# Optimization experiments

Hardware: AMD Instinct MI355X
Metric: run time of the kernel (lower is better)

Reference implementation:

```python
import jax, jax.numpy as jnp
import numpy as np

TAU = 0.07
MARGIN = 0.2
NUM_SPECIES = 64  # matches fill_max of species_ids


def _l2norm(x):
    return x / jnp.linalg.norm(x, axis=-1, keepdims=True)


def setup_inputs() -> dict:
    key = jax.random.key(0)
    k1, k2, k3 = jax.random.split(key, 3)
    B, D = 8192, 256
    species_embed = _l2norm(jax.random.normal(k1, (B, D), dtype=jnp.float32))
    text_embed = _l2norm(jax.random.normal(k2, (B, D), dtype=jnp.float32))
    species_ids = jax.random.randint(k3, (B,), 0, NUM_SPECIES, dtype=jnp.int32)
    return {"species_embed": species_embed, "text_embed": text_embed,
            "species_ids": species_ids}


def reference(species_embed, text_embed, species_ids):
    B = species_embed.shape[0]
    dtype = species_embed.dtype

    sim = species_embed @ text_embed.T                      # (B, B)
    same = species_ids[:, None] == species_ids[None, :]     # (B, B) bool, symmetric
    diag_sim = jnp.diagonal(sim)                            # (B,)

    # ---- intra-species symmetric InfoNCE (per-species CE, averaged over species)
    logits = sim / TAU
    neg_inf = jnp.finfo(dtype).min
    masked = jnp.where(same, logits, neg_inf)               # restrict to same-species cols
    diag_logit = diag_sim / TAU
    ce_v2t = jax.scipy.special.logsumexp(masked, axis=1) - diag_logit   # per-row CE
    ce_t2v = jax.scipy.special.logsumexp(masked.T, axis=1) - diag_logit # transpose: same mask is symmetric

    ones = jnp.ones((B,), dtype=dtype)
    counts = jax.ops.segment_sum(ones, species_ids, num_segments=NUM_SPECIES)          # group sizes
    seg_v2t = jax.ops.segment_sum(ce_v2t, species_ids, num_segments=NUM_SPECIES)
    seg_t2v = jax.ops.segment_sum(ce_t2v, species_ids, num_segments=NUM_SPECIES)
    valid_s = counts >= 2                                   # groups with <2 members skipped
    per_species = (seg_v2t + seg_t2v) / (2.0 * jnp.maximum(counts, 1.0))
    n_valid = jnp.maximum(jnp.sum(valid_s.astype(dtype)), 1.0)
    loss_infonce = jnp.sum(jnp.where(valid_s, per_species, 0.0)) / n_valid

    # ---- cross-species triplet (pos = mean same-species sim excl. self, neg = mean diff-species sim)
    same_f = same.astype(dtype)
    row_same_sum = jnp.sum(sim * same_f, axis=1)            # includes diagonal
    row_sum = jnp.sum(sim, axis=1)
    pos_cnt = jnp.sum(same_f, axis=1) - 1.0
    neg_cnt = B - jnp.sum(same_f, axis=1)
    pos_mean = (row_same_sum - diag_sim) / jnp.maximum(pos_cnt, 1.0)
    neg_mean = (row_sum - row_same_sum) / jnp.maximum(neg_cnt, 1.0)
    tri = jax.nn.relu(neg_mean - pos_mean + MARGIN)
    valid_i = (pos_cnt > 0) & (neg_cnt > 0)
    n_valid_i = jnp.maximum(jnp.sum(valid_i.astype(dtype)), 1.0)
    loss_triplet = jnp.sum(jnp.where(valid_i, tri, 0.0)) / n_valid_i

    return loss_infonce + loss_triplet
```

## Files before the change

kernel.cpp:

```cpp
#include <hip/hip_runtime.h>
#include <hip/hip_fp16.h>

#define TAU 0.07f
#define MARGIN 0.2f
#define NSPEC 64
#define BB 8192
#define DD 256

#define WS_SCALARS   0
#define WS_COUNTS    64
#define WS_OFFSETS   320
#define WS_LSEROW    1024
#define WS_LSECOL    33792
#define WS_TS        66560
#define WS_T         132096
#define WS_MEMBER    133120

typedef _Float16 half8 __attribute__((ext_vector_type(8)));
typedef float float4v __attribute__((ext_vector_type(4)));
typedef unsigned int uint4v __attribute__((ext_vector_type(4)));

__device__ __forceinline__ uint4v pack8(float4 a, float4 b) {
  half8 h;
  h[0] = (_Float16)a.x; h[1] = (_Float16)a.y; h[2] = (_Float16)a.z; h[3] = (_Float16)a.w;
  h[4] = (_Float16)b.x; h[5] = (_Float16)b.y; h[6] = (_Float16)b.z; h[7] = (_Float16)b.w;
  return __builtin_bit_cast(uint4v, h);
}

__device__ __forceinline__ float dot4(float4 a, float4 b) {
  return a.x * b.x + a.y * b.y + a.z * b.z + a.w * b.w;
}

__global__ void kA(const int* __restrict__ ids, char* __restrict__ ws) {
  int bid = blockIdx.x, tid = threadIdx.x;
  if (bid == 0) {
    int* counts_g = (int*)(ws + WS_COUNTS);
    int* offsets_g = (int*)(ws + WS_OFFSETS);
    int* memberList = (int*)(ws + WS_MEMBER);
    float* scalars = (float*)(ws + WS_SCALARS);
    __shared__ int cnt[NSPEC];
    __shared__ int off[NSPEC];
    if (tid < 8) ((unsigned*)scalars)[tid] = 0u;
    if (tid < NSPEC) cnt[tid] = 0;
    __syncthreads();
    int myS[8], myP[8];
    #pragma unroll
    for (int r = 0; r < 8; ++r) {
      int i = r * 1024 + tid;
      int s = ids[i];
      myS[r] = s;
      myP[r] = atomicAdd(&cnt[s], 1);
    }
    __syncthreads();
    if (tid < NSPEC) {
      int o = 0;
      for (int t = 0; t < NSPEC; ++t) o += (t < tid) ? cnt[t] : 0;
      off[tid] = o;
      offsets_g[tid] = o;
      int c = cnt[tid];
      counts_g[tid] = c;
      unsigned long long bv = __ballot(c >= 2);
      float nvi = (c >= 2 && c <= BB - 1) ? (float)c : 0.f;
      for (int o2 = 1; o2 < 64; o2 <<= 1) nvi += __shfl_xor(nvi, o2);
      if (tid == 0) {
        scalars[2] = (float)__popcll(bv);
        scalars[3] = nvi;
      }
    }
    __syncthreads();
    #pragma unroll
    for (int r = 0; r < 8; ++r) {
      int i = r * 1024 + tid;
      memberList[off[myS[r]] + myP[r]] = i;
    }
  } else {
    int b = bid - 1;
    if (tid < 258) {
      float4v z4 = {0.f, 0.f, 0.f, 0.f};
      *(float4v*)(ws + WS_LSEROW + b * 4128 + tid * 16) = z4;
    }
  }
}

__global__ void kB(const float* __restrict__ sp, const float* __restrict__ tx,
                   const int* __restrict__ counts, const int* __restrict__ offsets,
                   const int* __restrict__ memberList,
                   float* Ts, float* T, float* lseRow, float* lseCol) {
  __shared__ uint4v frag[1536];
  __shared__ int idx[192];
  int bid = blockIdx.x;
  int tid = threadIdx.x;

  if (bid >= 1024) {
    int b = bid - 1024;
    int d = tid;
    const float* base = tx + (b * 32) * DD + d;
    float acc = 0.f;
    #pragma unroll 8
    for (int rr = 0; rr < 32; ++rr) acc += base[rr * DD];
    atomicAdd(&T[d], acc);
    return;
  }
  if (bid >= 512) {
    int v2 = bid - 512;
    int s = v2 & 63, r = v2 >> 6;
    int m = counts[s], g0 = offsets[s];
    int k0 = (m * r) >> 3, k1e = (m * (r + 1)) >> 3;
    if (k0 >= k1e) return;
    int d = tid;
    float acc = 0.f;
    int k = k0;
    for (; k + 4 <= k1e; k += 4) {
      int i0 = memberList[g0 + k];
      int i1 = memberList[g0 + k + 1];
      int i2 = memberList[g0 + k + 2];
      int i3 = memberList[g0 + k + 3];
      float a0 = tx[i0 * DD + d];
      float a1 = tx[i1 * DD + d];
      float a2 = tx[i2 * DD + d];
      float a3 = tx[i3 * DD + d];
      acc += a0 + a1 + a2 + a3;
    }
    for (; k < k1e; ++k) acc += tx[memberList[g0 + k] * DD + d];
    atomicAdd(&Ts[s * DD + d], acc);
    return;
  }

  int s = bid & 63;
  int m = counts[s];
  int g0 = offsets[s];
  int lane = tid & 63, wv = tid >> 6;
  int quad = lane >> 4, cl = lane & 15;
  int rt0 = (bid >> 6) & 3, ct0 = (bid >> 8) & 1;

  for (int rt = rt0; rt * 64 < m; rt += 4) {
    for (int ct = ct0; ct * 128 < m; ct += 2) {
      __syncthreads();
      if (tid < 192) {
        int base = (tid < 64) ? (rt * 64 + tid) : (ct * 128 + (tid - 64));
        idx[tid] = (base < m) ? memberList[g0 + base] : -1;
      }
      __syncthreads();

      const float* srcB[6];
      bool val[6];
      int dst[6];
      float4 r0[6], r1[6];
      #pragma unroll
      for (int p = 0; p < 6; ++p) {
        int u = p * 256 + tid;
        int isB = u >= 512;
        int v = isB ? (u - 512) : u;
        int row = v >> 3, sub = v & 7;
        int ksl = sub >> 2, q = sub & 3;
        int ridx = idx[isB ? (64 + row) : row];
        val[p] = ridx >= 0;
        srcB[p] = (isB ? tx : sp) + (val[p] ? ridx : 0) * DD + ksl * 32 + q * 8;
        dst[p] = isB ? (512 + (ksl * 128 + row) * 4 + q)
                     : ((ksl * 64 + row) * 4 + q);
      }
      #pragma unroll
      for (int p = 0; p < 6; ++p) {
        r0[p] = *reinterpret_cast<const float4*>(srcB[p]);
        r1[p] = *reinterpret_cast<const float4*>(srcB[p] + 4);
      }

      float4v acc[8];
      #pragma unroll
      for (int cf = 0; cf < 8; ++cf) acc[cf] = (float4v){0.f, 0.f, 0.f, 0.f};

      for (int kc = 0; kc < 4; ++kc) {
        __syncthreads();
        uint4v z4 = (uint4v){0u, 0u, 0u, 0u};
        #pragma unroll
        for (int p = 0; p < 6; ++p)
          frag[dst[p]] = val[p] ? pack8(r0[p], r1[p]) : z4;
        __syncthreads();
        if (kc < 3) {
          #pragma unroll
          for (int p = 0; p < 6; ++p) {
            r0[p] = *reinterpret_cast<const float4*>(srcB[p] + (kc + 1) * 64);
            r1[p] = *reinterpret_cast<const float4*>(srcB[p] + (kc + 1) * 64 + 4);
          }
        }
        #pragma unroll
        for (int ksl = 0; ksl < 2; ++ksl) {
          half8 a = __builtin_bit_cast(half8, frag[(ksl * 64 + wv * 16 + cl) * 4 + quad]);
          #pragma unroll
          for (int cf = 0; cf < 8; ++cf) {
            half8 b = __builtin_bit_cast(half8, frag[512 + (ksl * 128 + cf * 16 + cl) * 4 + quad]);
            acc[cf] = __builtin_amdgcn_mfma_f32_16x16x32_f16(a, b, acc[cf], 0, 0, 0);
          }
        }
      }

      int riBase = rt * 64 + wv * 16 + quad * 4;
      float rowAcc[4] = {0.f, 0.f, 0.f, 0.f};
      #pragma unroll
      for (int cf = 0; cf < 8; ++cf) {
        int ci = ct * 128 + cf * 16 + cl;
        bool cv = ci < m;
        float colAcc = 0.f;
        #pragma unroll
        for (int reg = 0; reg < 4; ++reg) {
          bool rv = (riBase + reg) < m;
          float e = (rv && cv) ? __expf(acc[cf][reg] * (1.f / TAU)) : 0.f;
          rowAcc[reg] += e;
          colAcc += e;
        }
        colAcc += __shfl_xor(colAcc, 16);
        colAcc += __shfl_xor(colAcc, 32);
        if (quad == 0 && cv) atomicAdd(&lseCol[g0 + ci], colAcc);
      }
      #pragma unroll
      for (int reg = 0; reg < 4; ++reg) {
        float v = rowAcc[reg];
        v += __shfl_xor(v, 1);
        v += __shfl_xor(v, 2);
        v += __shfl_xor(v, 4);
        v += __shfl_xor(v, 8);
        if (cl == 0 && (riBase + reg) < m) atomicAdd(&lseRow[g0 + riBase + reg], v);
      }
    }
  }
}

__global__ void kC(const float* __restrict__ sp, const float* __restrict__ tx,
                   const int* __restrict__ ids, const int* __restrict__ counts,
                   const int* __restrict__ memberList,
                   const float* __restrict__ Ts, const float* __restrict__ T,
                   const float* __restrict__ lseRow, const float* __restrict__ lseCol,
                   float* scalars, float* out) {
  __shared__ float red[32];
  int tid = threadIdx.x;
  int gt = blockIdx.x * 1024 + tid;
  int g = gt >> 6, lane = gt & 63;
  int i = memberList[g];
  int s = ids[i];
  int m = counts[s];
  float4 a = *reinterpret_cast<const float4*>(sp + i * DD + lane * 4);
  float4 b = *reinterpret_cast<const float4*>(tx + i * DD + lane * 4);
  float4 c = *reinterpret_cast<const float4*>(Ts + s * DD + lane * 4);
  float4 tv = *reinterpret_cast<const float4*>(T + lane * 4);
  float dDiag = dot4(a, b);
  float dTs   = dot4(a, c);
  float dT    = dot4(a, tv);
  #pragma unroll
  for (int o = 1; o < 64; o <<= 1) {
    dDiag += __shfl_xor(dDiag, o);
    dTs   += __shfl_xor(dTs, o);
    dT    += __shfl_xor(dT, o);
  }
  if (lane == 0) {
    float term = 0.f, tri = 0.f;
    if (m >= 2) {
      term = (__logf(lseRow[g]) + __logf(lseCol[g]) - 2.f * dDiag * (1.f / TAU)) /
             (2.f * (float)m);
      float posMean = (dTs - dDiag) / fmaxf((float)(m - 1), 1.f);
      float negMean = (dT - dTs) / fmaxf((float)(BB - m), 1.f);
      if (m <= BB - 1) tri = fmaxf(negMean - posMean + MARGIN, 0.f);
    }
    int wv = tid >> 6;
    red[wv] = term;
    red[16 + wv] = tri;
  }
  __syncthreads();
  if (tid == 0) {
    float infoS = 0.f, triS = 0.f;
    #pragma unroll
    for (int w = 0; w < 16; ++w) { infoS += red[w]; triS += red[16 + w]; }
    atomicAdd(&scalars[1], infoS);
    atomicAdd(&scalars[0], triS);
    __threadfence();
    unsigned prev = atomicAdd((unsigned*)&scalars[4], 1u);
    if (prev == (unsigned)(gridDim.x - 1)) {
      float fi = atomicAdd(&scalars[1], 0.f);
      float ft = atomicAdd(&scalars[0], 0.f);
      float nv = scalars[2];
      float nvi = scalars[3];
      out[0] = fi / fmaxf(nv, 1.f) + ft / fmaxf(nvi, 1.f);
    }
  }
}

extern "C" void kernel_launch(void* const* d_in, const int* in_sizes, int n_in,
                              void* d_out, int out_size, void* d_ws, size_t ws_size,
                              hipStream_t stream) {
  const float* sp = (const float*)d_in[0];
  const float* tx = (const float*)d_in[1];
  const int* ids = (const int*)d_in[2];
  float* out = (float*)d_out;

  char* ws = (char*)d_ws;
  float* scalars = (float*)(ws + WS_SCALARS);
  int* counts = (int*)(ws + WS_COUNTS);
  int* offsets = (int*)(ws + WS_OFFSETS);
  float* lseRow = (float*)(ws + WS_LSEROW);
  float* lseCol = (float*)(ws + WS_LSECOL);
  float* Ts = (float*)(ws + WS_TS);
  float* T = (float*)(ws + WS_T);
  int* memberList = (int*)(ws + WS_MEMBER);

  kA<<<33, 1024, 0, stream>>>(ids, ws);
  kB<<<1280, 256, 0, stream>>>(sp, tx, counts, offsets, memberList,
                               Ts, T, lseRow, lseCol);
  kC<<<512, 1024, 0, stream>>>(sp, tx, ids, counts, memberList, Ts, T,
                               lseRow, lseCol, scalars, out);
}
```

Baseline: 111.3 us.

## Fuse three kernels into one persistent megakernel with flag-based inter-block sync

Merges the histogram/member-list, zeroing, masked GEMM-LSE, species-sum, total-sum and final reduction kernels into one launch where block ranges take roles and wait on global atomic flags and counters. It aims to remove kernel launch gaps and let independent work (e.g. the total text sum) overlap with the histogram phase. In exchange it relies on spin-waiting and co-residency/forward progress of blocks, and flags persisting across calls (flag1, flagZ0 never cleared) risk races with stale state on repeated invocations.

```diff
diff --git a/kernel.cpp b/kernel.cpp
--- a/kernel.cpp
+++ b/kernel.cpp
@@ -7,14 +7,30 @@
 #define BB 8192
 #define DD 256
 
-#define WS_SCALARS   0
-#define WS_COUNTS    64
-#define WS_OFFSETS   320
-#define WS_LSEROW    1024
-#define WS_LSECOL    33792
-#define WS_TS        66560
-#define WS_T         132096
-#define WS_MEMBER    133120
+#define MAGICZ 0x51u
+#define MAGIC1 0x1357A5C3u
+
+#define B_ZERO0   1
+#define B_K5      33
+#define B_K2      545
+#define B_T       1057
+#define B_KC      1313
+#define N_WORK2   1312u
+#define N_KC      2048
+#define N_TOTAL   3361
+
+#define WS_SCALARS 0
+#define WS_COUNTS  64
+#define WS_OFFSETS 320
+#define WS_FLAGZ0  576
+#define WS_ZCNT    580
+#define WS_FLAG1   584
+#define WS_DONE2   588
+#define WS_LSEROW  1024
+#define WS_LSECOL  33792
+#define WS_TS      66560
+#define WS_T       132096
+#define WS_MEMBER  133120
 
 typedef _Float16 half8 __attribute__((ext_vector_type(8)));
 typedef float float4v __attribute__((ext_vector_type(4)));
@@ -31,34 +47,62 @@
   return a.x * b.x + a.y * b.y + a.z * b.z + a.w * b.w;
 }
 
-__global__ void kA(const int* __restrict__ ids, char* __restrict__ ws) {
+__device__ __forceinline__ unsigned aload(unsigned* p) { return atomicAdd(p, 0u); }
+
+__device__ __forceinline__ void spin1(unsigned* p, unsigned v) {
+  if (threadIdx.x == 0) {
+    while (aload(p) != v) __builtin_amdgcn_s_sleep(8);
+  }
+  __syncthreads();
+}
+__device__ __forceinline__ void spin2(unsigned* p1, unsigned v1, unsigned* p2, unsigned v2) {
+  if (threadIdx.x == 0) {
+    while (aload(p1) != v1 || aload(p2) != v2) __builtin_amdgcn_s_sleep(8);
+  }
+  __syncthreads();
+}
+
+__global__ void __launch_bounds__(256)
+mega(const float* __restrict__ sp, const float* __restrict__ tx,
+     const int* __restrict__ ids, char* __restrict__ ws, float* __restrict__ out) {
+  float* scalars = (float*)(ws + WS_SCALARS);
+  int* counts = (int*)(ws + WS_COUNTS);
+  int* offsets = (int*)(ws + WS_OFFSETS);
+  unsigned* flagZ0 = (unsigned*)(ws + WS_FLAGZ0);
+  unsigned* zcnt = (unsigned*)(ws + WS_ZCNT);
+  unsigned* flag1 = (unsigned*)(ws + WS_FLAG1);
+  unsigned* done2 = (unsigned*)(ws + WS_DONE2);
+  float* lseRow = (float*)(ws + WS_LSEROW);
+  float* lseCol = (float*)(ws + WS_LSECOL);
+  float* Ts = (float*)(ws + WS_TS);
+  float* T = (float*)(ws + WS_T);
+  int* memberList = (int*)(ws + WS_MEMBER);
+
   int bid = blockIdx.x, tid = threadIdx.x;
+
+  __shared__ union {
+    struct { int cnt[NSPEC]; int cur[NSPEC]; } h;
+    struct { uint4v frag[1536]; int idx[192]; } k5;
+    float red[8];
+  } sm;
+
   if (bid == 0) {
-    int* counts_g = (int*)(ws + WS_COUNTS);
-    int* offsets_g = (int*)(ws + WS_OFFSETS);
-    int* memberList = (int*)(ws + WS_MEMBER);
-    float* scalars = (float*)(ws + WS_SCALARS);
-    __shared__ int cnt[NSPEC];
-    __shared__ int off[NSPEC];
+    if (tid == 0) { *zcnt = 0u; *done2 = 0u; }
     if (tid < 8) ((unsigned*)scalars)[tid] = 0u;
-    if (tid < NSPEC) cnt[tid] = 0;
-    __syncthreads();
-    int myS[8], myP[8];
+    if (tid < NSPEC) sm.h.cnt[tid] = 0;
+    __threadfence();
+    __syncthreads();
+    if (tid == 0) atomicExch(flagZ0, MAGICZ);
     #pragma unroll
-    for (int r = 0; r < 8; ++r) {
-      int i = r * 1024 + tid;
-      int s = ids[i];
-      myS[r] = s;
-      myP[r] = atomicAdd(&cnt[s], 1);
-    }
+    for (int r = 0; r < 32; ++r) atomicAdd(&sm.h.cnt[ids[r * 256 + tid]], 1);
     __syncthreads();
     if (tid < NSPEC) {
       int o = 0;
-      for (int t = 0; t < NSPEC; ++t) o += (t < tid) ? cnt[t] : 0;
-      off[tid] = o;
-      offsets_g[tid] = o;
-      int c = cnt[tid];
-      counts_g[tid] = c;
+      for (int t = 0; t < NSPEC; ++t) o += (t < tid) ? sm.h.cnt[t] : 0;
+      offsets[tid] = o;
+      sm.h.cur[tid] = o;
+      int c = sm.h.cnt[tid];
+      counts[tid] = c;
       unsigned long long bv = __ballot(c >= 2);
       float nvi = (c >= 2 && c <= BB - 1) ? (float)c : 0.f;
       for (int o2 = 1; o2 < 64; o2 <<= 1) nvi += __shfl_xor(nvi, o2);
@@ -69,216 +113,223 @@
     }
     __syncthreads();
     #pragma unroll
-    for (int r = 0; r < 8; ++r) {
-      int i = r * 1024 + tid;
-      memberList[off[myS[r]] + myP[r]] = i;
-    }
-  } else {
-    int b = bid - 1;
-    if (tid < 258) {
-      float4v z4 = {0.f, 0.f, 0.f, 0.f};
-      *(float4v*)(ws + WS_LSEROW + b * 4128 + tid * 16) = z4;
-    }
-  }
-}
-
-__global__ void kB(const float* __restrict__ sp, const float* __restrict__ tx,
-                   const int* __restrict__ counts, const int* __restrict__ offsets,
-                   const int* __restrict__ memberList,
-                   float* Ts, float* T, float* lseRow, float* lseCol) {
-  __shared__ uint4v frag[1536];
-  __shared__ int idx[192];
-  int bid = blockIdx.x;
-  int tid = threadIdx.x;
-
-  if (bid >= 1024) {
-    int b = bid - 1024;
+    for (int r = 0; r < 32; ++r) {
+      int i = r * 256 + tid;
+      int s = ids[i];
+      int pos = atomicAdd(&sm.h.cur[s], 1);
+      memberList[pos] = i;
+    }
+    __threadfence();
+    __syncthreads();
+    if (tid == 0) atomicExch(flag1, MAGIC1);
+    return;
+
+  } else if (bid < B_K5) {
+    spin1(flagZ0, MAGICZ);
+    int b = bid - B_ZERO0;
+    char* base = ws + WS_LSEROW + b * 4128;
+    float4v z4 = {0.f, 0.f, 0.f, 0.f};
+    *(float4v*)(base + tid * 16) = z4;
+    if (tid < 2) *(float4v*)(base + (256 + tid) * 16) = z4;
+    __threadfence();
+    __syncthreads();
+    if (tid == 0) atomicAdd(zcnt, 1u);
+    spin1(flag1, MAGIC1);
+    if (tid == 0) atomicAdd(done2, 1u);
+    return;
+
+  } else if (bid < B_K2) {
+    int v = bid - B_K5;
+    spin2(flag1, MAGIC1, zcnt, 32u);
+    int s = v & 63;
+    int m = counts[s];
+    int g0 = offsets[s];
+    int lane = tid & 63, wv = tid >> 6;
+    int quad = lane >> 4, cl = lane & 15;
+    int rt0 = (v >> 6) & 3, ct0 = (v >> 8) & 1;
+
+    for (int rt = rt0; rt * 64 < m; rt += 4) {
+      for (int ct = ct0; ct * 128 < m; ct += 2) {
+        __syncthreads();
+        if (tid < 192) {
+          int base = (tid < 64) ? (rt * 64 + tid) : (ct * 128 + (tid - 64));
+          sm.k5.idx[tid] = (base < m) ? memberList[g0 + base] : -1;
+        }
+        __syncthreads();
+
+        const float* srcB[6];
+        bool val[6];
+        int dst[6];
+        float4 r0[6], r1[6];
+        #pragma unroll
+        for (int p = 0; p < 6; ++p) {
+          int u = p * 256 + tid;
+          int isB = u >= 512;
+          int vv = isB ? (u - 512) : u;
+          int row = vv >> 3, sub = vv & 7;
+          int ksl = sub >> 2, q = sub & 3;
+          int ridx = sm.k5.idx[isB ? (64 + row) : row];
+          val[p] = ridx >= 0;
+          srcB[p] = (isB ? tx : sp) + (val[p] ? ridx : 0) * DD + ksl * 32 + q * 8;
+          dst[p] = isB ? (512 + (ksl * 128 + row) * 4 + q)
+                       : ((ksl * 64 + row) * 4 + q);
+        }
+        #pragma unroll
+        for (int p = 0; p < 6; ++p) {
+          r0[p] = *reinterpret_cast<const float4*>(srcB[p]);
+          r1[p] = *reinterpret_cast<const float4*>(srcB[p] + 4);
+        }
+
+        float4v acc[8];
+        #pragma unroll
+        for (int cf = 0; cf < 8; ++cf) acc[cf] = (float4v){0.f, 0.f, 0.f, 0.f};
+
+        for (int kc = 0; kc < 4; ++kc) {
+          __syncthreads();
+          uint4v z4 = (uint4v){0u, 0u, 0u, 0u};
+          #pragma unroll
+          for (int p = 0; p < 6; ++p)
+            sm.k5.frag[dst[p]] = val[p] ? pack8(r0[p], r1[p]) : z4;
+          __syncthreads();
+          if (kc < 3) {
+            #pragma unroll
+            for (int p = 0; p < 6; ++p) {
+              r0[p] = *reinterpret_cast<const float4*>(srcB[p] + (kc + 1) * 64);
+              r1[p] = *reinterpret_cast<const float4*>(srcB[p] + (kc + 1) * 64 + 4);
+            }
+          }
+          #pragma unroll
+          for (int ksl = 0; ksl < 2; ++ksl) {
+            half8 a = __builtin_bit_cast(half8, sm.k5.frag[(ksl * 64 + wv * 16 + cl) * 4 + quad]);
+            #pragma unroll
+            for (int cf = 0; cf < 8; ++cf) {
+              half8 b = __builtin_bit_cast(half8, sm.k5.frag[512 + (ksl * 128 + cf * 16 + cl) * 4 + quad]);
+              acc[cf] = __builtin_amdgcn_mfma_f32_16x16x32_f16(a, b, acc[cf], 0, 0, 0);
+            }
+          }
+        }
+
+        int riBase = rt * 64 + wv * 16 + quad * 4;
+        float rowAcc[4] = {0.f, 0.f, 0.f, 0.f};
+        #pragma unroll
+        for (int cf = 0; cf < 8; ++cf) {
+          int ci = ct * 128 + cf * 16 + cl;
+          bool cv = ci < m;
+          float colAcc = 0.f;
+          #pragma unroll
+          for (int reg = 0; reg < 4; ++reg) {
+            bool rv = (riBase + reg) < m;
+            float e = (rv && cv) ? __expf(acc[cf][reg] * (1.f / TAU)) : 0.f;
+            rowAcc[reg] += e;
+            colAcc += e;
+          }
+          colAcc += __shfl_xor(colAcc, 16);
+          colAcc += __shfl_xor(colAcc, 32);
+          if (quad == 0 && cv) atomicAdd(&lseCol[g0 + ci], colAcc);
+        }
+        #pragma unroll
+        for (int reg = 0; reg < 4; ++reg) {
+          float vv = rowAcc[reg];
+          vv += __shfl_xor(vv, 1);
+          vv += __shfl_xor(vv, 2);
+          vv += __shfl_xor(vv, 4);
+          vv += __shfl_xor(vv, 8);
+          if (cl == 0 && (riBase + reg) < m) atomicAdd(&lseRow[g0 + riBase + reg], vv);
+        }
+      }
+    }
+    __threadfence();
+    __syncthreads();
+    if (tid == 0) atomicAdd(done2, 1u);
+    return;
+
+  } else if (bid < B_T) {
+    int v2 = bid - B_K2;
+    spin2(flag1, MAGIC1, zcnt, 32u);
+    int s = v2 & 63, r = v2 >> 6;
+    int m = counts[s], g0 = offsets[s];
+    int k0 = (m * r) >> 3, k1e = (m * (r + 1)) >> 3;
+    if (k0 < k1e) {
+      int d = tid;
+      float acc = 0.f;
+      int k = k0;
+      for (; k + 4 <= k1e; k += 4) {
+        int i0 = memberList[g0 + k];
+        int i1 = memberList[g0 + k + 1];
+        int i2 = memberList[g0 + k + 2];
+        int i3 = memberList[g0 + k + 3];
+        acc += tx[i0 * DD + d] + tx[i1 * DD + d] + tx[i2 * DD + d] + tx[i3 * DD + d];
+      }
+      for (; k < k1e; ++k) acc += tx[memberList[g0 + k] * DD + d];
+      atomicAdd(&Ts[s * DD + d], acc);
+    }
+    __threadfence();
+    __syncthreads();
+    if (tid == 0) atomicAdd(done2, 1u);
+    return;
+
+  } else if (bid < B_KC) {
+    int b = bid - B_T;
     int d = tid;
     const float* base = tx + (b * 32) * DD + d;
     float acc = 0.f;
     #pragma unroll 8
     for (int rr = 0; rr < 32; ++rr) acc += base[rr * DD];
+    spin2(flag1, MAGIC1, zcnt, 32u);
     atomicAdd(&T[d], acc);
+    __threadfence();
+    __syncthreads();
+    if (tid == 0) atomicAdd(done2, 1u);
     return;
   }
-  if (bid >= 512) {
-    int v2 = bid - 512;
-    int s = v2 & 63, r = v2 >> 6;
-    int m = counts[s], g0 = offsets[s];
-    int k0 = (m * r) >> 3, k1e = (m * (r + 1)) >> 3;
-    if (k0 >= k1e) return;
-    int d = tid;
-    float acc = 0.f;
-    int k = k0;
-    for (; k + 4 <= k1e; k += 4) {
-      int i0 = memberList[g0 + k];
-      int i1 = memberList[g0 + k + 1];
-      int i2 = memberList[g0 + k + 2];
-      int i3 = memberList[g0 + k + 3];
-      float a0 = tx[i0 * DD + d];
-      float a1 = tx[i1 * DD + d];
-      float a2 = tx[i2 * DD + d];
-      float a3 = tx[i3 * DD + d];
-      acc += a0 + a1 + a2 + a3;
-    }
-    for (; k < k1e; ++k) acc += tx[memberList[g0 + k] * DD + d];
-    atomicAdd(&Ts[s * DD + d], acc);
-    return;
-  }
-
-  int s = bid & 63;
-  int m = counts[s];
-  int g0 = offsets[s];
-  int lane = tid & 63, wv = tid >> 6;
-  int quad = lane >> 4, cl = lane & 15;
-  int rt0 = (bid >> 6) & 3, ct0 = (bid >> 8) & 1;
-
-  for (int rt = rt0; rt * 64 < m; rt += 4) {
-    for (int ct = ct0; ct * 128 < m; ct += 2) {
-      __syncthreads();
-      if (tid < 192) {
-        int base = (tid < 64) ? (rt * 64 + tid) : (ct * 128 + (tid - 64));
-        idx[tid] = (base < m) ? memberList[g0 + base] : -1;
-      }
-      __syncthreads();
-
-      const float* srcB[6];
-      bool val[6];
-      int dst[6];
-      float4 r0[6], r1[6];
-      #pragma unroll
-      for (int p = 0; p < 6; ++p) {
-        int u = p * 256 + tid;
-        int isB = u >= 512;
-        int v = isB ? (u - 512) : u;
-        int row = v >> 3, sub = v & 7;
-        int ksl = sub >> 2, q = sub & 3;
-        int ridx = idx[isB ? (64 + row) : row];
-        val[p] = ridx >= 0;
-        srcB[p] = (isB ? tx : sp) + (val[p] ? ridx : 0) * DD + ksl * 32 + q * 8;
-        dst[p] = isB ? (512 + (ksl * 128 + row) * 4 + q)
-                     : ((ksl * 64 + row) * 4 + q);
-      }
-      #pragma unroll
-      for (int p = 0; p < 6; ++p) {
-        r0[p] = *reinterpret_cast<const float4*>(srcB[p]);
-        r1[p] = *reinterpret_cast<const float4*>(srcB[p] + 4);
-      }
-
-      float4v acc[8];
-      #pragma unroll
-      for (int cf = 0; cf < 8; ++cf) acc[cf] = (float4v){0.f, 0.f, 0.f, 0.f};
-
-      for (int kc = 0; kc < 4; ++kc) {
-        __syncthreads();
-        uint4v z4 = (uint4v){0u, 0u, 0u, 0u};
-        #pragma unroll
-        for (int p = 0; p < 6; ++p)
-          frag[dst[p]] = val[p] ? pack8(r0[p], r1[p]) : z4;
-        __syncthreads();
-        if (kc < 3) {
-          #pragma unroll
-          for (int p = 0; p < 6; ++p) {
-            r0[p] = *reinterpret_cast<const float4*>(srcB[p] + (kc + 1) * 64);
-            r1[p] = *reinterpret_cast<const float4*>(srcB[p] + (kc + 1) * 64 + 4);
-          }
-        }
-        #pragma unroll
-        for (int ksl = 0; ksl < 2; ++ksl) {
-          half8 a = __builtin_bit_cast(half8, frag[(ksl * 64 + wv * 16 + cl) * 4 + quad]);
-          #pragma unroll
-          for (int cf = 0; cf < 8; ++cf) {
-            half8 b = __builtin_bit_cast(half8, frag[512 + (ksl * 128 + cf * 16 + cl) * 4 + quad]);
-            acc[cf] = __builtin_amdgcn_mfma_f32_16x16x32_f16(a, b, acc[cf], 0, 0, 0);
-          }
-        }
-      }
-
-      int riBase = rt * 64 + wv * 16 + quad * 4;
-      float rowAcc[4] = {0.f, 0.f, 0.f, 0.f};
-      #pragma unroll
-      for (int cf = 0; cf < 8; ++cf) {
-        int ci = ct * 128 + cf * 16 + cl;
-        bool cv = ci < m;
-        float colAcc = 0.f;
-        #pragma unroll
-        for (int reg = 0; reg < 4; ++reg) {
-          bool rv = (riBase + reg) < m;
-          float e = (rv && cv) ? __expf(acc[cf][reg] * (1.f / TAU)) : 0.f;
-          rowAcc[reg] += e;
-          colAcc += e;
-        }
-        colAcc += __shfl_xor(colAcc, 16);
-        colAcc += __shfl_xor(colAcc, 32);
-        if (quad == 0 && cv) atomicAdd(&lseCol[g0 + ci], colAcc);
-      }
-      #pragma unroll
-      for (int reg = 0; reg < 4; ++reg) {
-        float v = rowAcc[reg];
-        v += __shfl_xor(v, 1);
-        v += __shfl_xor(v, 2);
-        v += __shfl_xor(v, 4);
-        v += __shfl_xor(v, 8);
-        if (cl == 0 && (riBase + reg) < m) atomicAdd(&lseRow[g0 + riBase + reg], v);
-      }
-    }
-  }
-}
-
-__global__ void kC(const float* __restrict__ sp, const float* __restrict__ tx,
-                   const int* __restrict__ ids, const int* __restrict__ counts,
-                   const int* __restrict__ memberList,
-                   const float* __restrict__ Ts, const float* __restrict__ T,
-                   const float* __restrict__ lseRow, const float* __restrict__ lseCol,
-                   float* scalars, float* out) {
-  __shared__ float red[32];
-  int tid = threadIdx.x;
-  int gt = blockIdx.x * 1024 + tid;
-  int g = gt >> 6, lane = gt & 63;
-  int i = memberList[g];
-  int s = ids[i];
-  int m = counts[s];
-  float4 a = *reinterpret_cast<const float4*>(sp + i * DD + lane * 4);
-  float4 b = *reinterpret_cast<const float4*>(tx + i * DD + lane * 4);
-  float4 c = *reinterpret_cast<const float4*>(Ts + s * DD + lane * 4);
-  float4 tv = *reinterpret_cast<const float4*>(T + lane * 4);
-  float dDiag = dot4(a, b);
-  float dTs   = dot4(a, c);
-  float dT    = dot4(a, tv);
-  #pragma unroll
-  for (int o = 1; o < 64; o <<= 1) {
-    dDiag += __shfl_xor(dDiag, o);
-    dTs   += __shfl_xor(dTs, o);
-    dT    += __shfl_xor(dT, o);
-  }
-  if (lane == 0) {
-    float term = 0.f, tri = 0.f;
-    if (m >= 2) {
-      term = (__logf(lseRow[g]) + __logf(lseCol[g]) - 2.f * dDiag * (1.f / TAU)) /
-             (2.f * (float)m);
-      float posMean = (dTs - dDiag) / fmaxf((float)(m - 1), 1.f);
-      float negMean = (dT - dTs) / fmaxf((float)(BB - m), 1.f);
-      if (m <= BB - 1) tri = fmaxf(negMean - posMean + MARGIN, 0.f);
-    }
-    int wv = tid >> 6;
-    red[wv] = term;
-    red[16 + wv] = tri;
-  }
-  __syncthreads();
-  if (tid == 0) {
-    float infoS = 0.f, triS = 0.f;
+
+  {
+    int cb = bid - B_KC;
+    spin1(flag1, MAGIC1);
+    int wv = tid >> 6, lane = tid & 63;
+    int g = cb * 4 + wv;
+    int i = memberList[g];
+    int s = ids[i];
+    int m = counts[s];
+    float4 a = *reinterpret_cast<const float4*>(sp + i * DD + lane * 4);
+    float4 b = *reinterpret_cast<const float4*>(tx + i * DD + lane * 4);
+    spin1(done2, N_WORK2);
+    float4 c = *reinterpret_cast<const float4*>(Ts + s * DD + lane * 4);
+    float4 tv = *reinterpret_cast<const float4*>(T + lane * 4);
+    float dDiag = dot4(a, b);
+    float dTs   = dot4(a, c);
+    float dT    = dot4(a, tv);
     #pragma unroll
-    for (int w = 0; w < 16; ++w) { infoS += red[w]; triS += red[16 + w]; }
-    atomicAdd(&scalars[1], infoS);
-    atomicAdd(&scalars[0], triS);
-    __threadfence();
-    unsigned prev = atomicAdd((unsigned*)&scalars[4], 1u);
-    if (prev == (unsigned)(gridDim.x - 1)) {
-      float fi = atomicAdd(&scalars[1], 0.f);
-      float ft = atomicAdd(&scalars[0], 0.f);
-      float nv = scalars[2];
-      float nvi = scalars[3];
-      out[0] = fi / fmaxf(nv, 1.f) + ft / fmaxf(nvi, 1.f);
+    for (int o = 1; o < 64; o <<= 1) {
+      dDiag += __shfl_xor(dDiag, o);
+      dTs   += __shfl_xor(dTs, o);
+      dT    += __shfl_xor(dT, o);
+    }
+    if (lane == 0) {
+      float term = 0.f, tri = 0.f;
+      if (m >= 2) {
+        term = (__logf(lseRow[g]) + __logf(lseCol[g]) - 2.f * dDiag * (1.f / TAU)) /
+               (2.f * (float)m);
+        float posMean = (dTs - dDiag) / fmaxf((float)(m - 1), 1.f);
+        float negMean = (dT - dTs) / fmaxf((float)(BB - m), 1.f);
+        if (m <= BB - 1) tri = fmaxf(negMean - posMean + MARGIN, 0.f);
+      }
+      sm.red[wv] = term;
+      sm.red[4 + wv] = tri;
+    }
+    __syncthreads();
+    if (tid == 0) {
+      atomicAdd(&scalars[1], sm.red[0] + sm.red[1] + sm.red[2] + sm.red[3]);
+      atomicAdd(&scalars[0], sm.red[4] + sm.red[5] + sm.red[6] + sm.red[7]);
+      __threadfence();
+      unsigned prev = atomicAdd(&((unsigned*)scalars)[4], 1u);
+      if (prev == (unsigned)(N_KC - 1)) {
+        float fi = atomicAdd(&scalars[1], 0.f);
+        float ft = atomicAdd(&scalars[0], 0.f);
+        float nv = scalars[2];
+        float nvi = scalars[3];
+        out[0] = fi / fmaxf(nv, 1.f) + ft / fmaxf(nvi, 1.f);
+      }
     }
   }
 }
@@ -290,20 +341,7 @@
   const float* tx = (const float*)d_in[1];
   const int* ids = (const int*)d_in[2];
   float* out = (float*)d_out;
-
   char* ws = (char*)d_ws;
-  float* scalars = (float*)(ws + WS_SCALARS);
-  int* counts = (int*)(ws + WS_COUNTS);
-  int* offsets = (int*)(ws + WS_OFFSETS);
-  float* lseRow = (float*)(ws + WS_LSEROW);
-  float* lseCol = (float*)(ws + WS_LSECOL);
-  float* Ts = (float*)(ws + WS_TS);
-  float* T = (float*)(ws + WS_T);
-  int* memberList = (int*)(ws + WS_MEMBER);
-
-  kA<<<33, 1024, 0, stream>>>(ids, ws);
-  kB<<<1280, 256, 0, stream>>>(sp, tx, counts, offsets, memberList,
-                               Ts, T, lseRow, lseCol);
-  kC<<<512, 1024, 0, stream>>>(sp, tx, ids, counts, memberList, Ts, T,
-                               lseRow, lseCol, scalars, out);
-}
+
+  mega<<<N_TOTAL, 256, 0, stream>>>(sp, tx, ids, ws, out);
+}
```

Result: slower. 345.7 us (+210.6%).
